# Performance work log

Hardware: AMD Instinct MI355X
Metric: run time of the kernel (lower is better)

## Reference

```python
import jax, jax.numpy as jnp
import numpy as np

NCONF = 500      # configurations in batch
APC = 40         # atoms per configuration
NATOMS = NCONF * APC
ND = 64          # descriptor length
H = 128          # hidden width
NPAIRS = NATOMS * 20   # neighbor pairs
NDERIV = 3 * NPAIRS    # one row per (pair, cartesian axis)


def _mlp(x, W1, b1, W2, b2, W3, b3):
    h = jax.nn.sigmoid(x @ W1 + b1)
    h = jax.nn.sigmoid(h @ W2 + b2)
    return h @ W3 + b3  # [natoms, 1] per-atom energies


def setup_inputs() -> dict:
    key = jax.random.key(0)
    ks = jax.random.split(key, 8)
    x = jax.random.normal(ks[0], (NATOMS, ND), jnp.float32)
    xd = jax.random.normal(ks[1], (NDERIV, ND), jnp.float32)
    # contiguous config ids per atom
    indices = jnp.repeat(jnp.arange(NCONF, dtype=jnp.int32), APC)
    atoms_per_structure = jnp.full((NCONF,), APC, jnp.int32)
    types = jnp.zeros((NATOMS,), jnp.int32)
    # per-pair atom/neighbor ids, repeated for x/y/z rows
    pair_i = jax.random.randint(ks[2], (NPAIRS,), 0, NATOMS, jnp.int32)
    pair_j = jax.random.randint(ks[3], (NPAIRS,), 0, NATOMS, jnp.int32)
    unique_i = jnp.repeat(pair_i, 3)
    unique_j = jnp.repeat(pair_j, 3)
    axis = jnp.tile(jnp.arange(3, dtype=jnp.int32), NPAIRS)
    xd_indx = jnp.stack([jnp.repeat(pair_i, 3), jnp.repeat(pair_j, 3), axis], axis=1)
    # MLP parameters (fan-in scaled)
    W1 = jax.random.normal(ks[4], (ND, H), jnp.float32) / np.sqrt(ND)
    W2 = jax.random.normal(ks[5], (H, H), jnp.float32) / np.sqrt(H)
    W3 = jax.random.normal(ks[6], (H, 1), jnp.float32) / np.sqrt(H)
    b1 = jnp.zeros((H,), jnp.float32)
    b2 = jnp.zeros((H,), jnp.float32)
    b3 = jnp.zeros((1,), jnp.float32)
    return {"x": x, "xd": xd, "indices": indices,
            "atoms_per_structure": atoms_per_structure, "types": types,
            "xd_indx": xd_indx, "unique_i": unique_i, "unique_j": unique_j,
            "W1": W1, "b1": b1, "W2": W2, "b2": b2, "W3": W3, "b3": b3,
            "natoms": NATOMS}


def reference(x, xd, indices, atoms_per_structure, types, xd_indx,
              unique_i, unique_j, W1, b1, W2, b2, W3, b3, natoms):
    nconf = atoms_per_structure.shape[0]
    per_atom_energies = _mlp(x, W1, b1, W2, b2, W3, b3)[:, 0]  # [natoms]
    # energy: contract per-atom energies into per-config totals
    predicted_energy_total = jax.ops.segment_sum(per_atom_energies, indices,
                                                 num_segments=nconf)
    # dE/dD: gradient of total energy w.r.t. descriptors (vjp with ones)
    dEdD = jax.grad(lambda xx: jnp.sum(_mlp(xx, W1, b1, W2, b2, W3, b3)))(x)
    # gather dE/dD at neighbor rows, multiply by dD/dR, reduce over descriptor dim
    per_row = jnp.einsum('nd,nd->n', xd, dEdD[unique_i])  # [NDERIV]
    # scatter-add into (atom j, axis); equivalent to torch's three index_add_
    # followed by sum over descriptor dim and interleaved (fx,fy,fz) flatten
    axis = xd_indx[:, 2]
    flat_idx = unique_j * 3 + axis
    predicted_forces = jax.ops.segment_sum(per_row, flat_idx,
                                           num_segments=3 * natoms)
    return (predicted_energy_total, predicted_forces)
```

## Files before the change

### kernel.cpp

```cpp
#include <hip/hip_runtime.h>

typedef float f32x4 __attribute__((ext_vector_type(4)));
typedef __bf16 bf16x8 __attribute__((ext_vector_type(8)));
typedef unsigned int u32x4 __attribute__((ext_vector_type(4)));

#define TT 32

#define PW1_HI   0
#define PW1_LO   8192
#define PW2_HI   16384
#define PW2_LO   32768
#define PW2T_HI  49152
#define PW2T_LO  65536
#define PW1T_HI  81920
#define PW1T_LO  90112
#define PW_SLOTS 49152

__global__ void zero_kernel(float* __restrict__ p, int n) {
    int i = blockIdx.x * blockDim.x + threadIdx.x;
    if (i < n) p[i] = 0.f;
}

__device__ __forceinline__ void bf16split(float x, unsigned short& hi, unsigned short& lo) {
    unsigned u = __float_as_uint(x);
    unsigned r = (u + 0x7FFFu + ((u >> 16) & 1u)) >> 16;
    hi = (unsigned short)r;
    float hf = __uint_as_float(r << 16);
    unsigned u2 = __float_as_uint(x - hf);
    unsigned r2 = (u2 + 0x7FFFu + ((u2 >> 16) & 1u)) >> 16;
    lo = (unsigned short)r2;
}

__device__ __forceinline__ void split2(float a, float b, unsigned& hw, unsigned& lw) {
    unsigned ua = __float_as_uint(a);
    unsigned ra = (ua + 0x7FFFu + ((ua >> 16) & 1u)) >> 16;
    unsigned ua2 = __float_as_uint(a - __uint_as_float(ra << 16));
    unsigned la = (ua2 + 0x7FFFu + ((ua2 >> 16) & 1u)) >> 16;
    unsigned ub = __float_as_uint(b);
    unsigned rb = (ub + 0x7FFFu + ((ub >> 16) & 1u)) >> 16;
    unsigned ub2 = __float_as_uint(b - __uint_as_float(rb << 16));
    unsigned lb = (ub2 + 0x7FFFu + ((ub2 >> 16) & 1u)) >> 16;
    hw = ra | (rb << 16);
    lw = la | (lb << 16);
}

__global__ void pack_weights(const float* __restrict__ W1, const float* __restrict__ W2,
                             unsigned short* __restrict__ pw) {
    int s = blockIdx.x * blockDim.x + threadIdx.x;
    if (s >= PW_SLOTS) return;
    int slot, NS, hiOff, loOff; const float* src; bool tr;
    if (s < 8192)       { slot = s;         NS = 8; hiOff = PW1_HI;  loOff = PW1_LO;  tr = false; src = W1; }
    else if (s < 24576) { slot = s - 8192;  NS = 8; hiOff = PW2_HI;  loOff = PW2_LO;  tr = false; src = W2; }
    else if (s < 40960) { slot = s - 24576; NS = 8; hiOff = PW2T_HI; loOff = PW2T_LO; tr = true;  src = W2; }
    else                { slot = s - 40960; NS = 4; hiOff = PW1T_HI; loOff = PW1T_LO; tr = true;  src = W1; }
    int j = slot & 7, lane = (slot >> 3) & 63, rest = slot >> 9;
    int ns = rest % NS, ks = rest / NS;
    int k = ks * 32 + ((lane >> 4) & 3) * 8 + j;
    int n = ns * 16 + (lane & 15);
    float v = tr ? src[n * 128 + k] : src[k * 128 + n];
    unsigned short hi, lo;
    bf16split(v, hi, lo);
    pw[hiOff + slot] = hi;
    pw[loOff + slot] = lo;
}

__global__ __launch_bounds__(256, 2) void mlp_mfma(
    const float* __restrict__ x,
    const float* __restrict__ b1, const float* __restrict__ b2,
    const float* __restrict__ W3, const float* __restrict__ b3,
    const int* __restrict__ indices,
    const unsigned short* __restrict__ pw,
    float* __restrict__ energy, float* __restrict__ dEdD, int natoms)
{
    __shared__ float xs[TT * 64];
    __shared__ float h1s[TT * 128];
    __shared__ float g2s[TT * 128];

    const int tid = threadIdx.x;
    const int l   = tid & 63;
    const int w   = tid >> 6;
    const int col = l & 15;
    const int rg  = l >> 4;
    const int msub = w >> 1;
    const int half = w & 1;
    const int a0 = blockIdx.x * TT;
    const int mrow = msub * 16 + col;

    #pragma unroll
    for (int p = 0; p < 2; ++p) {
        int idx = tid + p * 256;
        int r = idx >> 4, c = idx & 15;
        int a = a0 + r;
        f32x4 v = {0.f, 0.f, 0.f, 0.f};
        if (a < natoms) v = *(const f32x4*)(x + (size_t)a * 64 + c * 4);
        *(f32x4*)(xs + r * 64 + ((c ^ (r & 7)) << 2)) = v;
    }
    __syncthreads();

    auto loadA = [&](const float* buf, int stride, int kbase, bf16x8& ah, bf16x8& al) {
        int key = mrow & 7;
        int c0 = kbase >> 2;
        f32x4 f0 = *(const f32x4*)(buf + mrow * stride + (((c0    ) ^ key) << 2));
        f32x4 f1 = *(const f32x4*)(buf + mrow * stride + (((c0 + 1) ^ key) << 2));
        u32x4 H, L;
        unsigned hw, lw;
        split2(f0[0], f0[1], hw, lw); H[0] = hw; L[0] = lw;
        split2(f0[2], f0[3], hw, lw); H[1] = hw; L[1] = lw;
        split2(f1[0], f1[1], hw, lw); H[2] = hw; L[2] = lw;
        split2(f1[2], f1[3], hw, lw); H[3] = hw; L[3] = lw;
        ah = __builtin_bit_cast(bf16x8, H);
        al = __builtin_bit_cast(bf16x8, L);
    };
    auto loadB = [&](int hiOff, int loOff, int NS, int ks, int nsub, bf16x8& bh, bf16x8& bl) {
        size_t idx = ((size_t)(ks * NS + nsub) * 64 + l) * 8;
        bh = __builtin_bit_cast(bf16x8, *(const u32x4*)(pw + hiOff + idx));
        bl = __builtin_bit_cast(bf16x8, *(const u32x4*)(pw + loOff + idx));
    };

    bf16x8 ah[4], al[4];

    loadA(xs, 64, 0 * 32 + rg * 8, ah[0], al[0]);
    loadA(xs, 64, 1 * 32 + rg * 8, ah[1], al[1]);
    for (int ns = 0; ns < 4; ++ns) {
        int nsub = half * 4 + ns, n0 = nsub * 16;
        float bv = b1[n0 + col];
        f32x4 acc = {bv, bv, bv, bv};
        #pragma unroll
        for (int ks = 0; ks < 2; ++ks) {
            bf16x8 bh, bl; loadB(PW1_HI, PW1_LO, 8, ks, nsub, bh, bl);
            acc = __builtin_amdgcn_mfma_f32_16x16x32_bf16(ah[ks], bh, acc, 0, 0, 0);
            acc = __builtin_amdgcn_mfma_f32_16x16x32_bf16(al[ks], bh, acc, 0, 0, 0);
            acc = __builtin_amdgcn_mfma_f32_16x16x32_bf16(ah[ks], bl, acc, 0, 0, 0);
        }
        #pragma unroll
        for (int r2 = 0; r2 < 4; ++r2) {
            int m = msub * 16 + rg * 4 + r2, k = n0 + col;
            float h = 1.f / (1.f + expf(-acc[r2]));
            h1s[m * 128 + ((((k >> 2)) ^ (m & 7)) << 2) + (k & 3)] = h;
        }
    }
    __syncthreads();

    #pragma unroll
    for (int ks = 0; ks < 4; ++ks) loadA(h1s, 128, ks * 32 + rg * 8, ah[ks], al[ks]);
    float e[4] = {0.f, 0.f, 0.f, 0.f};
    for (int ns = 0; ns < 4; ++ns) {
        int nsub = half * 4 + ns, n0 = nsub * 16;
        float bv = b2[n0 + col];
        f32x4 acc = {bv, bv, bv, bv};
        #pragma unroll
        for (int ks = 0; ks < 4; ++ks) {
            bf16x8 bh, bl; loadB(PW2_HI, PW2_LO, 8, ks, nsub, bh, bl);
            acc = __builtin_amdgcn_mfma_f32_16x16x32_bf16(ah[ks], bh, acc, 0, 0, 0);
            acc = __builtin_amdgcn_mfma_f32_16x16x32_bf16(al[ks], bh, acc, 0, 0, 0);
            acc = __builtin_amdgcn_mfma_f32_16x16x32_bf16(ah[ks], bl, acc, 0, 0, 0);
        }
        float w3v = W3[n0 + col];
        #pragma unroll
        for (int r2 = 0; r2 < 4; ++r2) {
            float h2 = 1.f / (1.f + expf(-acc[r2]));
            e[r2] += h2 * w3v;
            float g = w3v * h2 * (1.f - h2);
            int m = msub * 16 + rg * 4 + r2, k = n0 + col;
            g2s[m * 128 + ((((k >> 2)) ^ (m & 7)) << 2) + (k & 3)] = g;
        }
    }
    #pragma unroll
    for (int r2 = 0; r2 < 4; ++r2) {
        float v = e[r2];
        v += __shfl_xor(v, 1); v += __shfl_xor(v, 2);
        v += __shfl_xor(v, 4); v += __shfl_xor(v, 8);
        e[r2] = v;
    }
    if (col == 0) {
        float b3v = (half == 0) ? b3[0] : 0.f;
        #pragma unroll
        for (int r2 = 0; r2 < 4; ++r2) {
            int a = a0 + msub * 16 + rg * 4 + r2;
            if (a < natoms) atomicAdd(&energy[indices[a]], e[r2] + b3v);
        }
    }
    __syncthreads();

    #pragma unroll
    for (int ks = 0; ks < 4; ++ks) loadA(g2s, 128, ks * 32 + rg * 8, ah[ks], al[ks]);
    for (int ns = 0; ns < 4; ++ns) {
        int nsub = half * 4 + ns, n0 = nsub * 16;
        f32x4 acc = {0.f, 0.f, 0.f, 0.f};
        #pragma unroll
        for (int ks = 0; ks < 4; ++ks) {
            bf16x8 bh, bl; loadB(PW2T_HI, PW2T_LO, 8, ks, nsub, bh, bl);
            acc = __builtin_amdgcn_mfma_f32_16x16x32_bf16(ah[ks], bh, acc, 0, 0, 0);
            acc = __builtin_amdgcn_mfma_f32_16x16x32_bf16(al[ks], bh, acc, 0, 0, 0);
            acc = __builtin_amdgcn_mfma_f32_16x16x32_bf16(ah[ks], bl, acc, 0, 0, 0);
        }
        #pragma unroll
        for (int r2 = 0; r2 < 4; ++r2) {
            int m = msub * 16 + rg * 4 + r2, k = n0 + col;
            int off = m * 128 + ((((k >> 2)) ^ (m & 7)) << 2) + (k & 3);
            float hv = h1s[off];
            h1s[off] = acc[r2] * hv * (1.f - hv);
        }
    }
    __syncthreads();

    #pragma unroll
    for (int ks = 0; ks < 4; ++ks) loadA(h1s, 128, ks * 32 + rg * 8, ah[ks], al[ks]);
    for (int ns = 0; ns < 2; ++ns) {
        int nsub = half * 2 + ns, n0 = nsub * 16;
        f32x4 acc = {0.f, 0.f, 0.f, 0.f};
        #pragma unroll
        for (int ks = 0; ks < 4; ++ks) {
            bf16x8 bh, bl; loadB(PW1T_HI, PW1T_LO, 4, ks, nsub, bh, bl);
            acc = __builtin_amdgcn_mfma_f32_16x16x32_bf16(ah[ks], bh, acc, 0, 0, 0);
            acc = __builtin_amdgcn_mfma_f32_16x16x32_bf16(al[ks], bh, acc, 0, 0, 0);
            acc = __builtin_amdgcn_mfma_f32_16x16x32_bf16(ah[ks], bl, acc, 0, 0, 0);
        }
        #pragma unroll
        for (int r2 = 0; r2 < 4; ++r2) {
            int a = a0 + msub * 16 + rg * 4 + r2;
            if (a < natoms) dEdD[(size_t)a * 64 + n0 + col] = acc[r2];
        }
    }
}

__global__ __launch_bounds__(256) void force_kernel(
    const float* __restrict__ xd,
    const int* __restrict__ unique_i, const int* __restrict__ unique_j,
    const float* __restrict__ dEdD,
    float* __restrict__ forces, int nderiv)
{
    const int tid = threadIdx.x;
    const int lane = tid & 63;
    const int wib = tid >> 6;
    const int gwave = blockIdx.x * 4 + wib;
    const int nwaves = gridDim.x * 4;
    const int sub = lane >> 4;
    const int t = lane & 15;
    const int ngroups = (nderiv + 3) >> 2;

    for (int g = gwave; g < ngroups; g += nwaves) {
        const int r = g * 4 + sub;
        float p = 0.f;
        int jdst = 0, ax = 0;
        const bool valid = (r < nderiv);
        if (valid) {
            const int ai = unique_i[r];
            const float4 v = ((const float4*)(xd   + (size_t)r  * 64))[t];
            const float4 wv = ((const float4*)(dEdD + (size_t)ai * 64))[t];
            p = v.x * wv.x + v.y * wv.y + v.z * wv.z + v.w * wv.w;
            jdst = unique_j[r];
            ax = r % 3;
        }
        p += __shfl_xor(p, 1);
        p += __shfl_xor(p, 2);
        p += __shfl_xor(p, 4);
        p += __shfl_xor(p, 8);
        if (t == 0 && valid) atomicAdd(&forces[jdst * 3 + ax], p);
    }
}

extern "C" void kernel_launch(void* const* d_in, const int* in_sizes, int n_in,
                              void* d_out, int out_size, void* d_ws, size_t ws_size,
                              hipStream_t stream) {
    const float* x        = (const float*)d_in[0];
    const float* xd       = (const float*)d_in[1];
    const int*   indices  = (const int*)d_in[2];
    const int*   unique_i = (const int*)d_in[6];
    const int*   unique_j = (const int*)d_in[7];
    const float* W1       = (const float*)d_in[8];
    const float* b1       = (const float*)d_in[9];
    const float* W2       = (const float*)d_in[10];
    const float* b2       = (const float*)d_in[11];
    const float* W3       = (const float*)d_in[12];
    const float* b3       = (const float*)d_in[13];

    const int natoms = in_sizes[2];
    const int nconf  = in_sizes[3];
    const int nderiv = in_sizes[6];

    float* out    = (float*)d_out;
    float* energy = out;
    float* forces = out + nconf;
    float* dEdD   = (float*)d_ws;
    unsigned short* pw = (unsigned short*)((char*)d_ws + (size_t)natoms * 64 * 4);

    const int ntiles = (natoms + TT - 1) / TT;

    zero_kernel<<<(out_size + 255) / 256, 256, 0, stream>>>(out, out_size);
    pack_weights<<<(PW_SLOTS + 255) / 256, 256, 0, stream>>>(W1, W2, pw);
    mlp_mfma<<<ntiles, 256, 0, stream>>>(x, b1, b2, W3, b3, indices, pw,
                                         energy, dEdD, natoms);
    force_kernel<<<2048, 256, 0, stream>>>(xd, unique_i, unique_j, dEdD,
                                           forces, nderiv);
}
```

Before: 140.5 us.

## Store MLP activations pre-split as bf16 hi/lo in MFMA fragment layout with 512-thread blocks

Activations in shared memory are now kept as pre-split bf16 hi/lo pairs, laid out directly in the MFMA A-fragment order. Each A operand becomes a single 16-byte LDS load instead of two float loads followed by repeated split work. The block grows to 8 waves, each covering a quarter of the N columns, which spreads the per-tile work and is meant to raise parallelism. In exchange it adds scalar 2-byte LDS stores, a reconstruction of h from its bf16 parts in the backward pass, and higher register and launch-bound demands.

```diff
diff --git a/kernel.cpp b/kernel.cpp
--- a/kernel.cpp
+++ b/kernel.cpp
@@ -3,6 +3,7 @@
 typedef float f32x4 __attribute__((ext_vector_type(4)));
 typedef __bf16 bf16x8 __attribute__((ext_vector_type(8)));
 typedef unsigned int u32x4 __attribute__((ext_vector_type(4)));
+typedef unsigned int u32x2 __attribute__((ext_vector_type(2)));
 
 #define TT 32
 
@@ -64,7 +65,7 @@
     pw[loOff + slot] = lo;
 }
 
-__global__ __launch_bounds__(256, 2) void mlp_mfma(
+__global__ __launch_bounds__(512, 4) void mlp_mfma(
     const float* __restrict__ x,
     const float* __restrict__ b1, const float* __restrict__ b2,
     const float* __restrict__ W3, const float* __restrict__ b3,
@@ -72,88 +73,94 @@
     const unsigned short* __restrict__ pw,
     float* __restrict__ energy, float* __restrict__ dEdD, int natoms)
 {
-    __shared__ float xs[TT * 64];
-    __shared__ float h1s[TT * 128];
-    __shared__ float g2s[TT * 128];
+    __shared__ __align__(16) unsigned short xsH[2 * 2 * 64 * 8];
+    __shared__ __align__(16) unsigned short xsL[2 * 2 * 64 * 8];
+    __shared__ __align__(16) unsigned short h1H[4 * 2 * 64 * 8];
+    __shared__ __align__(16) unsigned short h1L[4 * 2 * 64 * 8];
+    __shared__ __align__(16) unsigned short g2H[4 * 2 * 64 * 8];
+    __shared__ __align__(16) unsigned short g2L[4 * 2 * 64 * 8];
 
     const int tid = threadIdx.x;
     const int l   = tid & 63;
     const int w   = tid >> 6;
     const int col = l & 15;
     const int rg  = l >> 4;
-    const int msub = w >> 1;
-    const int half = w & 1;
+    const int msub = w >> 2;
+    const int nq   = w & 3;
     const int a0 = blockIdx.x * TT;
-    const int mrow = msub * 16 + col;
-
-    #pragma unroll
-    for (int p = 0; p < 2; ++p) {
-        int idx = tid + p * 256;
-        int r = idx >> 4, c = idx & 15;
+
+    {
+        int r = tid >> 4, c4 = tid & 15;
         int a = a0 + r;
         f32x4 v = {0.f, 0.f, 0.f, 0.f};
-        if (a < natoms) v = *(const f32x4*)(x + (size_t)a * 64 + c * 4);
-        *(f32x4*)(xs + r * 64 + ((c ^ (r & 7)) << 2)) = v;
+        if (a < natoms) v = *(const f32x4*)(x + (size_t)a * 64 + c4 * 4);
+        unsigned h01, l01, h23, l23;
+        split2(v[0], v[1], h01, l01);
+        split2(v[2], v[3], h23, l23);
+        int ks = c4 >> 3;
+        int lane2 = (r & 15) + (((c4 >> 1) & 3) << 4);
+        int j2 = (c4 * 4) & 7;
+        int off = (((ks * 2 + (r >> 4)) * 64 + lane2) << 3) + j2;
+        *(u32x2*)(xsH + off) = (u32x2){h01, h23};
+        *(u32x2*)(xsL + off) = (u32x2){l01, l23};
     }
     __syncthreads();
 
-    auto loadA = [&](const float* buf, int stride, int kbase, bf16x8& ah, bf16x8& al) {
-        int key = mrow & 7;
-        int c0 = kbase >> 2;
-        f32x4 f0 = *(const f32x4*)(buf + mrow * stride + (((c0    ) ^ key) << 2));
-        f32x4 f1 = *(const f32x4*)(buf + mrow * stride + (((c0 + 1) ^ key) << 2));
-        u32x4 H, L;
-        unsigned hw, lw;
-        split2(f0[0], f0[1], hw, lw); H[0] = hw; L[0] = lw;
-        split2(f0[2], f0[3], hw, lw); H[1] = hw; L[1] = lw;
-        split2(f1[0], f1[1], hw, lw); H[2] = hw; L[2] = lw;
-        split2(f1[2], f1[3], hw, lw); H[3] = hw; L[3] = lw;
-        ah = __builtin_bit_cast(bf16x8, H);
-        al = __builtin_bit_cast(bf16x8, L);
+    auto loadAB = [&](const unsigned short* pH, const unsigned short* pL,
+                      int ks, bf16x8& ah, bf16x8& al) {
+        int off = ((ks * 2 + msub) * 64 + l) << 3;
+        ah = __builtin_bit_cast(bf16x8, *(const u32x4*)(pH + off));
+        al = __builtin_bit_cast(bf16x8, *(const u32x4*)(pL + off));
     };
     auto loadB = [&](int hiOff, int loOff, int NS, int ks, int nsub, bf16x8& bh, bf16x8& bl) {
-        size_t idx = ((size_t)(ks * NS + nsub) * 64 + l) * 8;
+        int idx = ((ks * NS + nsub) * 64 + l) << 3;
         bh = __builtin_bit_cast(bf16x8, *(const u32x4*)(pw + hiOff + idx));
         bl = __builtin_bit_cast(bf16x8, *(const u32x4*)(pw + loOff + idx));
     };
-
-    bf16x8 ah[4], al[4];
-
-    loadA(xs, 64, 0 * 32 + rg * 8, ah[0], al[0]);
-    loadA(xs, 64, 1 * 32 + rg * 8, ah[1], al[1]);
-    for (int ns = 0; ns < 4; ++ns) {
-        int nsub = half * 4 + ns, n0 = nsub * 16;
+    auto dstOff = [&](int r2, int nsub, int cl) {
+        int ks2 = nsub >> 1;
+        int lane2 = (rg * 4 + r2) + (((nsub * 2 + (cl >> 3)) & 3) << 4);
+        return (((ks2 * 2 + msub) * 64 + lane2) << 3) + (cl & 7);
+    };
+
+    #pragma unroll
+    for (int ns = 0; ns < 2; ++ns) {
+        int nsub = nq * 2 + ns, n0 = nsub * 16;
         float bv = b1[n0 + col];
         f32x4 acc = {bv, bv, bv, bv};
         #pragma unroll
         for (int ks = 0; ks < 2; ++ks) {
-            bf16x8 bh, bl; loadB(PW1_HI, PW1_LO, 8, ks, nsub, bh, bl);
-            acc = __builtin_amdgcn_mfma_f32_16x16x32_bf16(ah[ks], bh, acc, 0, 0, 0);
-            acc = __builtin_amdgcn_mfma_f32_16x16x32_bf16(al[ks], bh, acc, 0, 0, 0);
-            acc = __builtin_amdgcn_mfma_f32_16x16x32_bf16(ah[ks], bl, acc, 0, 0, 0);
-        }
-        #pragma unroll
-        for (int r2 = 0; r2 < 4; ++r2) {
-            int m = msub * 16 + rg * 4 + r2, k = n0 + col;
+            bf16x8 ah, al, bh, bl;
+            loadAB(xsH, xsL, ks, ah, al);
+            loadB(PW1_HI, PW1_LO, 8, ks, nsub, bh, bl);
+            acc = __builtin_amdgcn_mfma_f32_16x16x32_bf16(ah, bh, acc, 0, 0, 0);
+            acc = __builtin_amdgcn_mfma_f32_16x16x32_bf16(al, bh, acc, 0, 0, 0);
+            acc = __builtin_amdgcn_mfma_f32_16x16x32_bf16(ah, bl, acc, 0, 0, 0);
+        }
+        #pragma unroll
+        for (int r2 = 0; r2 < 4; ++r2) {
             float h = 1.f / (1.f + expf(-acc[r2]));
-            h1s[m * 128 + ((((k >> 2)) ^ (m & 7)) << 2) + (k & 3)] = h;
+            unsigned short hi, lo; bf16split(h, hi, lo);
+            int off = dstOff(r2, nsub, col);
+            h1H[off] = hi; h1L[off] = lo;
         }
     }
     __syncthreads();
 
+    float e[4] = {0.f, 0.f, 0.f, 0.f};
     #pragma unroll
-    for (int ks = 0; ks < 4; ++ks) loadA(h1s, 128, ks * 32 + rg * 8, ah[ks], al[ks]);
-    float e[4] = {0.f, 0.f, 0.f, 0.f};
-    for (int ns = 0; ns < 4; ++ns) {
-        int nsub = half * 4 + ns, n0 = nsub * 16;
+    for (int ns = 0; ns < 2; ++ns) {
+        int nsub = nq * 2 + ns, n0 = nsub * 16;
         float bv = b2[n0 + col];
         f32x4 acc = {bv, bv, bv, bv};
         #pragma unroll
         for (int ks = 0; ks < 4; ++ks) {
-            bf16x8 bh, bl; loadB(PW2_HI, PW2_LO, 8, ks, nsub, bh, bl);
-            acc = __builtin_amdgcn_mfma_f32_16x16x32_bf16(ah[ks], bh, acc, 0, 0, 0);
-            acc = __builtin_amdgcn_mfma_f32_16x16x32_bf16(al[ks], bh, acc, 0, 0, 0);
-            acc = __builtin_amdgcn_mfma_f32_16x16x32_bf16(ah[ks], bl, acc, 0, 0, 0);
+            bf16x8 ah, al, bh, bl;
+            loadAB(h1H, h1L, ks, ah, al);
+            loadB(PW2_HI, PW2_LO, 8, ks, nsub, bh, bl);
+            acc = __builtin_amdgcn_mfma_f32_16x16x32_bf16(ah, bh, acc, 0, 0, 0);
+            acc = __builtin_amdgcn_mfma_f32_16x16x32_bf16(al, bh, acc, 0, 0, 0);
+            acc = __builtin_amdgcn_mfma_f32_16x16x32_bf16(ah, bl, acc, 0, 0, 0);
         }
         float w3v = W3[n0 + col];
         #pragma unroll
@@ -161,8 +168,9 @@
             float h2 = 1.f / (1.f + expf(-acc[r2]));
             e[r2] += h2 * w3v;
             float g = w3v * h2 * (1.f - h2);
-            int m = msub * 16 + rg * 4 + r2, k = n0 + col;
-            g2s[m * 128 + ((((k >> 2)) ^ (m & 7)) << 2) + (k & 3)] = g;
+            unsigned short hi, lo; bf16split(g, hi, lo);
+            int off = dstOff(r2, nsub, col);
+            g2H[off] = hi; g2L[off] = lo;
         }
     }
     #pragma unroll
@@ -173,7 +181,7 @@
         e[r2] = v;
     }
     if (col == 0) {
-        float b3v = (half == 0) ? b3[0] : 0.f;
+        float b3v = (nq == 0) ? b3[0] : 0.f;
         #pragma unroll
         for (int r2 = 0; r2 < 4; ++r2) {
             int a = a0 + msub * 16 + rg * 4 + r2;
@@ -183,38 +191,41 @@
     __syncthreads();
 
     #pragma unroll
-    for (int ks = 0; ks < 4; ++ks) loadA(g2s, 128, ks * 32 + rg * 8, ah[ks], al[ks]);
-    for (int ns = 0; ns < 4; ++ns) {
-        int nsub = half * 4 + ns, n0 = nsub * 16;
+    for (int ns = 0; ns < 2; ++ns) {
+        int nsub = nq * 2 + ns;
         f32x4 acc = {0.f, 0.f, 0.f, 0.f};
         #pragma unroll
         for (int ks = 0; ks < 4; ++ks) {
-            bf16x8 bh, bl; loadB(PW2T_HI, PW2T_LO, 8, ks, nsub, bh, bl);
-            acc = __builtin_amdgcn_mfma_f32_16x16x32_bf16(ah[ks], bh, acc, 0, 0, 0);
-            acc = __builtin_amdgcn_mfma_f32_16x16x32_bf16(al[ks], bh, acc, 0, 0, 0);
-            acc = __builtin_amdgcn_mfma_f32_16x16x32_bf16(ah[ks], bl, acc, 0, 0, 0);
-        }
-        #pragma unroll
-        for (int r2 = 0; r2 < 4; ++r2) {
-            int m = msub * 16 + rg * 4 + r2, k = n0 + col;
-            int off = m * 128 + ((((k >> 2)) ^ (m & 7)) << 2) + (k & 3);
-            float hv = h1s[off];
-            h1s[off] = acc[r2] * hv * (1.f - hv);
+            bf16x8 ah, al, bh, bl;
+            loadAB(g2H, g2L, ks, ah, al);
+            loadB(PW2T_HI, PW2T_LO, 8, ks, nsub, bh, bl);
+            acc = __builtin_amdgcn_mfma_f32_16x16x32_bf16(ah, bh, acc, 0, 0, 0);
+            acc = __builtin_amdgcn_mfma_f32_16x16x32_bf16(al, bh, acc, 0, 0, 0);
+            acc = __builtin_amdgcn_mfma_f32_16x16x32_bf16(ah, bl, acc, 0, 0, 0);
+        }
+        #pragma unroll
+        for (int r2 = 0; r2 < 4; ++r2) {
+            int off = dstOff(r2, nsub, col);
+            float h = __uint_as_float((unsigned)h1H[off] << 16)
+                    + __uint_as_float((unsigned)h1L[off] << 16);
+            float dz = acc[r2] * h * (1.f - h);
+            unsigned short hi, lo; bf16split(dz, hi, lo);
+            h1H[off] = hi; h1L[off] = lo;
         }
     }
     __syncthreads();
 
-    #pragma unroll
-    for (int ks = 0; ks < 4; ++ks) loadA(h1s, 128, ks * 32 + rg * 8, ah[ks], al[ks]);
-    for (int ns = 0; ns < 2; ++ns) {
-        int nsub = half * 2 + ns, n0 = nsub * 16;
+    {
+        int nsub = nq, n0 = nq * 16;
         f32x4 acc = {0.f, 0.f, 0.f, 0.f};
         #pragma unroll
         for (int ks = 0; ks < 4; ++ks) {
-            bf16x8 bh, bl; loadB(PW1T_HI, PW1T_LO, 4, ks, nsub, bh, bl);
-            acc = __builtin_amdgcn_mfma_f32_16x16x32_bf16(ah[ks], bh, acc, 0, 0, 0);
-            acc = __builtin_amdgcn_mfma_f32_16x16x32_bf16(al[ks], bh, acc, 0, 0, 0);
-            acc = __builtin_amdgcn_mfma_f32_16x16x32_bf16(ah[ks], bl, acc, 0, 0, 0);
+            bf16x8 ah, al, bh, bl;
+            loadAB(h1H, h1L, ks, ah, al);
+            loadB(PW1T_HI, PW1T_LO, 4, ks, nsub, bh, bl);
+            acc = __builtin_amdgcn_mfma_f32_16x16x32_bf16(ah, bh, acc, 0, 0, 0);
+            acc = __builtin_amdgcn_mfma_f32_16x16x32_bf16(al, bh, acc, 0, 0, 0);
+            acc = __builtin_amdgcn_mfma_f32_16x16x32_bf16(ah, bl, acc, 0, 0, 0);
         }
         #pragma unroll
         for (int r2 = 0; r2 < 4; ++r2) {
@@ -289,7 +300,7 @@
 
     zero_kernel<<<(out_size + 255) / 256, 256, 0, stream>>>(out, out_size);
     pack_weights<<<(PW_SLOTS + 255) / 256, 256, 0, stream>>>(W1, W2, pw);
-    mlp_mfma<<<ntiles, 256, 0, stream>>>(x, b1, b2, W3, b3, indices, pw,
+    mlp_mfma<<<ntiles, 512, 0, stream>>>(x, b1, b2, W3, b3, indices, pw,
                                          energy, dEdD, natoms);
     force_kernel<<<2048, 256, 0, stream>>>(xd, unique_i, unique_j, dEdD,
                                            forces, nderiv);
```

Measured after the change: 171.6 us. +22.2%, slower.
